# Optimization experiments

Hardware: AMD Instinct MI355X
Metric: run time of the kernel (lower is better)

## Reference

```python
import jax, jax.numpy as jnp
import numpy as np

B, N, K = 2, 8192, 9
IN_CH, FEAT_CH, COST_CH = 64, 128, 64

def _bn(x, p, eps=1e-5):
    # eval-mode BatchNorm; p is [4, C] = (gamma, beta, running_mean, running_var)
    sh = (1, -1) + (1,) * (x.ndim - 2)
    g, b, m, v = (p[i].reshape(sh) for i in range(4))
    return (x - m) / jnp.sqrt(v + eps) * g + b

def _c1(x, w, b):
    # Conv1d kernel 1: x [B,C,N], w [O,C]
    return jnp.einsum('oc,bcn->bon', w, x) + b[None, :, None]

def _forward(xyz, points, cost_volume, feats, flow,
             w0, b0, bn0, w1, b1, bn1,
             wz, bz, wr, br, wq, bq,
             w2a, b2a, w2b, b2b, wfc, bfc,
             rw0, rbn0, rw1, rbn1, rw2, rbn2,
             cw0, cbn0, cw1, cbn1, cw2, cbn2):
    lrelu = lambda t: jax.nn.leaky_relu(t, 0.1)
    # --- self-KNN on xyz ---
    xt = jnp.transpose(xyz, (0, 2, 1))                   # B N 3
    sq = jnp.sum(xt * xt, -1)                            # B N
    d2 = sq[:, :, None] + sq[:, None, :] - 2.0 * jnp.einsum('bnd,bmd->bnm', xt, xt)
    idx = jax.lax.top_k(-d2, K)[1]                       # B N K (nearest incl. self)
    # --- grouping_operation: gather neighbor features ---
    np0 = jnp.concatenate([cost_volume, flow], 1)        # B (cost_ch+3) N
    g = jax.vmap(lambda p, i: p[:, i])(np0, idx)         # B C N K
    # --- Conv2d(1x1)+BN+LeakyReLU stack ---
    g = lrelu(_bn(jnp.einsum('oc,bcnk->bonk', w0, g) + b0[None, :, None, None], bn0))
    g = lrelu(_bn(jnp.einsum('oc,bcnk->bonk', w1, g) + b1[None, :, None, None], bn1))
    h = jnp.max(g, -1)                                   # max over neighbors -> B 128 N
    # --- ConvGRU(x=feats, h) with 1x1 Conv1d gates ---
    hx = jnp.concatenate([h, feats], 1)
    z = jax.nn.sigmoid(_c1(hx, wz, bz))
    r = jax.nn.sigmoid(_c1(hx, wr, br))
    q = jnp.tanh(_c1(jnp.concatenate([r * h, feats], 1), wq, bq))
    h = (1.0 - z) * h + z * q
    # --- Conv1d MLP head ---
    x = jnp.concatenate([points, h], 1)                  # B (in_ch+128) N
    x = lrelu(_c1(x, w2a, b2a))
    x = lrelu(_c1(x, w2b, b2b))
    re_flow = _c1(x, wfc, bfc)                           # B 3 N
    # --- prob regnets (Conv1d no-bias + BN + ReLU) ---
    def reg(y, ws, ps):
        for w, p in zip(ws, ps):
            y = jax.nn.relu(_bn(jnp.einsum('oc,bcn->bon', w, y), p))
        return y
    refine = reg(x, [rw0, rw1, rw2], [rbn0, rbn1, rbn2])         # B 1 N
    coarse = reg(cost_volume, [cw0, cw1, cw2], [cbn0, cbn1, cbn2])
    re_flow = coarse * flow + refine * re_flow
    return x, jnp.clip(re_flow, -20.0, 20.0)

def setup_inputs():
    key = jax.random.key(0)
    ks = iter(jax.random.split(key, 80))
    nrm = lambda shape, s=1.0: jax.random.normal(next(ks), shape, jnp.float32) * s
    def bnp(C):
        g = jax.random.uniform(next(ks), (C,), jnp.float32) + 0.5
        b = nrm((C,), 0.1); m = nrm((C,), 0.1)
        v = jax.random.uniform(next(ks), (C,), jnp.float32) + 0.5
        return jnp.stack([g, b, m, v])
    z = lambda C: jnp.zeros((C,), jnp.float32)
    return dict(
        xyz=nrm((B, 3, N)), points=nrm((B, IN_CH, N)), cost_volume=nrm((B, COST_CH, N)),
        feats=nrm((B, FEAT_CH, N)), flow=nrm((B, 3, N), 0.1),
        w0=nrm((128, COST_CH + 3), 0.05), b0=z(128), bn0=bnp(128),
        w1=nrm((128, 128), 0.05), b1=z(128), bn1=bnp(128),
        wz=nrm((128, 256), 0.05), bz=z(128), wr=nrm((128, 256), 0.05), br=z(128),
        wq=nrm((128, 256), 0.05), bq=z(128),
        w2a=nrm((128, IN_CH + 128), 0.05), b2a=z(128), w2b=nrm((64, 128), 0.05), b2b=z(64),
        wfc=nrm((3, 64), 0.05), bfc=z(3),
        rw0=nrm((64, 64), 0.05), rbn0=bnp(64), rw1=nrm((64, 64), 0.05), rbn1=bnp(64),
        rw2=nrm((1, 64), 0.05), rbn2=bnp(1),
        cw0=nrm((64, COST_CH), 0.05), cbn0=bnp(64), cw1=nrm((64, 64), 0.05), cbn1=bnp(64),
        cw2=nrm((1, 64), 0.05), cbn2=bnp(1),
    )

def reference(xyz, points, cost_volume, feats, flow, w0, b0, bn0, w1, b1, bn1, wz, bz, wr, br, wq, bq, w2a, b2a, w2b, b2b, wfc, bfc, rw0, rbn0, rw1, rbn1, rw2, rbn2, cw0, cbn0, cw1, cbn1, cw2, cbn2):
    return _forward(xyz, points, cost_volume, feats, flow, w0, b0, bn0, w1, b1, bn1, wz, bz, wr, br, wq, bq, w2a, b2a, w2b, b2b, wfc, bfc, rw0, rbn0, rw1, rbn1, rw2, rbn2, cw0, cbn0, cw1, cbn1, cw2, cbn2)
```

## Files before the change

### kernel.cpp

```cpp
#include <hip/hip_runtime.h>
#include <math.h>

typedef __bf16 bf16;
typedef __bf16 bf16x4 __attribute__((ext_vector_type(4)));
typedef __bf16 bf16x8 __attribute__((ext_vector_type(8)));
typedef float f32x4 __attribute__((ext_vector_type(4)));

#define NPTS 8192
#define MTOT 16384

static __device__ __forceinline__ float b2f(bf16 x) { return (float)x; }
static __device__ __forceinline__ bf16  f2b(float x) { return (bf16)x; }

__global__ void diag_k(float* out, float code)
{
    if (threadIdx.x == 0 && blockIdx.x == 0) out[0] = code;
}

static __device__ __forceinline__ void pack_body(bf16 (*tile)[68],
                                                 const float* __restrict__ src, int Csrc,
                                                 bf16* __restrict__ dst, int ldd,
                                                 int nb, int cb, int b)
{
    const int t = threadIdx.x;
#pragma unroll
    for (int i = 0; i < 8; ++i) {
        int id = t + i * 256;
        int c = id >> 6, n = id & 63;
        int cc = cb + c;
        bf16 v = (bf16)0.0f;
        if (cc < Csrc) v = f2b(src[(size_t)(b * Csrc + cc) * NPTS + nb + n]);
        tile[c][n] = v;
    }
    __syncthreads();
#pragma unroll
    for (int i = 0; i < 8; ++i) {
        int id = t + i * 256;
        int n = id >> 5, c = id & 31;
        dst[(size_t)(b * NPTS + nb + n) * ldd + cb + c] = tile[c][n];
    }
}

static __device__ __forceinline__ float tau32(unsigned u)
{
    unsigned m = 0x80000000u | (unsigned)(~((int)u >> 31));
    return __uint_as_float(u ^ m);
}

static __device__ __forceinline__ unsigned dpp_shr1_u(unsigned x)
{
    return (unsigned)__builtin_amdgcn_update_dpp(0, (int)x, 0x111, 0xf, 0xf, true);
}
static __device__ __forceinline__ int dpp_shr1_i(int x)
{
    return __builtin_amdgcn_update_dpp(0, x, 0x111, 0xf, 0xf, true);
}

static __device__ __forceinline__ void mm32(
    f32x4 (&acc)[2][2],
    const bf16* A1, int lda1, int row01, int K1,
    const bf16* A2, int lda2, int row02,
    const bf16* W, int ldw, int K, int ob)
{
    const int lane = threadIdx.x & 63;
    const int q = lane >> 4, r = lane & 15;
    const bf16* Wp = W + (size_t)(ob + r) * ldw + q * 8;
    for (int k = 0; k < K; k += 32) {
        const bf16* Ap; int ld;
        if (k < K1) { ld = lda1; Ap = A1 + (size_t)(row01 + r) * lda1 + q * 8 + k; }
        else        { ld = lda2; Ap = A2 + (size_t)(row02 + r) * lda2 + q * 8 + (k - K1); }
        bf16x8 bv0 = *(const bf16x8*)(Wp + k);
        bf16x8 bv1 = *(const bf16x8*)(Wp + 16 * ldw + k);
        bf16x8 a0 = *(const bf16x8*)(Ap);
        bf16x8 a1 = *(const bf16x8*)(Ap + 16 * ld);
        acc[0][0] = __builtin_amdgcn_mfma_f32_16x16x32_bf16(a0, bv0, acc[0][0], 0, 0, 0);
        acc[1][0] = __builtin_amdgcn_mfma_f32_16x16x32_bf16(a1, bv0, acc[1][0], 0, 0, 0);
        acc[0][1] = __builtin_amdgcn_mfma_f32_16x16x32_bf16(a0, bv1, acc[0][1], 0, 0, 0);
        acc[1][1] = __builtin_amdgcn_mfma_f32_16x16x32_bf16(a1, bv1, acc[1][1], 0, 0, 0);
    }
}

static __device__ __forceinline__ void mm32x2(
    f32x4 (&acc)[2][2], f32x4 (&acc2)[2][2],
    const bf16* A1, int lda1, int row01, int K1,
    const bf16* A2, int lda2, int row02,
    const bf16* Wa, const bf16* Wb, int ldw, int K, int ob)
{
    const int lane = threadIdx.x & 63;
    const int q = lane >> 4, r = lane & 15;
    const bf16* Wpa = Wa + (size_t)(ob + r) * ldw + q * 8;
    const bf16* Wpb = Wb + (size_t)(ob + r) * ldw + q * 8;
    for (int k = 0; k < K; k += 32) {
        const bf16* Ap; int ld;
        if (k < K1) { ld = lda1; Ap = A1 + (size_t)(row01 + r) * lda1 + q * 8 + k; }
        else        { ld = lda2; Ap = A2 + (size_t)(row02 + r) * lda2 + q * 8 + (k - K1); }
        bf16x8 a0 = *(const bf16x8*)(Ap);
        bf16x8 a1 = *(const bf16x8*)(Ap + 16 * ld);
        bf16x8 ba0 = *(const bf16x8*)(Wpa + k);
        bf16x8 ba1 = *(const bf16x8*)(Wpa + 16 * ldw + k);
        bf16x8 bb0 = *(const bf16x8*)(Wpb + k);
        bf16x8 bb1 = *(const bf16x8*)(Wpb + 16 * ldw + k);
        acc[0][0]  = __builtin_amdgcn_mfma_f32_16x16x32_bf16(a0, ba0, acc[0][0], 0, 0, 0);
        acc[1][0]  = __builtin_amdgcn_mfma_f32_16x16x32_bf16(a1, ba0, acc[1][0], 0, 0, 0);
        acc[0][1]  = __builtin_amdgcn_mfma_f32_16x16x32_bf16(a0, ba1, acc[0][1], 0, 0, 0);
        acc[1][1]  = __builtin_amdgcn_mfma_f32_16x16x32_bf16(a1, ba1, acc[1][1], 0, 0, 0);
        acc2[0][0] = __builtin_amdgcn_mfma_f32_16x16x32_bf16(a0, bb0, acc2[0][0], 0, 0, 0);
        acc2[1][0] = __builtin_amdgcn_mfma_f32_16x16x32_bf16(a1, bb0, acc2[1][0], 0, 0, 0);
        acc2[0][1] = __builtin_amdgcn_mfma_f32_16x16x32_bf16(a0, bb1, acc2[0][1], 0, 0, 0);
        acc2[1][1] = __builtin_amdgcn_mfma_f32_16x16x32_bf16(a1, bb1, acc2[1][1], 0, 0, 0);
    }
}

static __device__ __forceinline__ void zacc(f32x4 (&acc)[2][2])
{
    f32x4 z = {0.f, 0.f, 0.f, 0.f};
    acc[0][0] = z; acc[0][1] = z; acc[1][0] = z; acc[1][1] = z;
}

__global__ __launch_bounds__(256) void pack_a(
    const float* __restrict__ w0, const float* __restrict__ w1,
    const float* __restrict__ wz, const float* __restrict__ wr,
    const float* __restrict__ wq, const float* __restrict__ w2a,
    const float* __restrict__ w2b, const float* __restrict__ rw0,
    const float* __restrict__ rw1, const float* __restrict__ cw0,
    const float* __restrict__ cw1,
    const float* __restrict__ cost, const float* __restrict__ flow,
    bf16* __restrict__ w0p, bf16* __restrict__ wts,
    bf16* __restrict__ CV, bf16* __restrict__ FL)
{
    __shared__ __align__(16) bf16 tile[32][68];
    const int bx = blockIdx.x;
    if (bx < 48) {
        int id = bx * 256 + threadIdx.x;
        if (id < 128 * 96) {
            int o = id / 96, c = id - o * 96;
            w0p[id] = (c < 67) ? f2b(w0[o * 67 + c]) : (bf16)0.0f;
        }
    } else if (bx < 688) {
        int id = (bx - 48) * 256 + threadIdx.x;
        if (id < 163840) {
            const float* s; int off;
            if (id < 16384)       { s = w1;  off = 0; }
            else if (id < 49152)  { s = wz;  off = 16384; }
            else if (id < 81920)  { s = wr;  off = 49152; }
            else if (id < 114688) { s = wq;  off = 81920; }
            else if (id < 139264) { s = w2a; off = 114688; }
            else if (id < 147456) { s = w2b; off = 139264; }
            else if (id < 151552) { s = rw0; off = 147456; }
            else if (id < 155648) { s = rw1; off = 151552; }
            else if (id < 159744) { s = cw0; off = 155648; }
            else                  { s = cw1; off = 159744; }
            wts[id] = f2b(s[id - off]);
        }
    } else if (bx < 1200) {
        int l = bx - 688, x = l & 127, r2 = l >> 7;
        pack_body(tile, cost, 64, CV, 64, x * 64, (r2 & 1) * 32, r2 >> 1);
    } else {
        int l = bx - 1200, x = l & 127, b = l >> 7;
        pack_body(tile, flow, 3, FL, 32, x * 64, 0, b);
    }
}

__global__ __launch_bounds__(256, 5) void knn_conv_packb(
    const float* __restrict__ xyz, const float* __restrict__ feats,
    const float* __restrict__ points,
    const bf16* __restrict__ CV, const bf16* __restrict__ FL,
    const bf16* __restrict__ W0p, const bf16* __restrict__ W1,
    const float* __restrict__ b0, const float* __restrict__ bn0,
    const float* __restrict__ b1, const float* __restrict__ bn1,
    bf16* __restrict__ FE, bf16* __restrict__ PT,
    bf16* __restrict__ P2, int* __restrict__ idxg)
{
    __shared__ __align__(16) char smem[16384];
    const int bx = blockIdx.x;
    if (bx < 4096) {
        float4* pts = (float4*)smem;
        const int t = threadIdx.x, lane = t & 63, w = t >> 6;
        const int qid = bx * 4 + w, b = qid >> 13;
        const float* X = xyz + b * 3 * NPTS;
        const int n = qid & (NPTS - 1);
        const float qx = X[n], qy = X[NPTS + n], qz = X[2 * NPTS + n];
        const float qsq = qx * qx + qy * qy + qz * qz;

        unsigned kkd = 0xFFFFFFFFu;
        int      idd = 0;
        float tau = __builtin_inff();

        for (int ch = 0; ch < 8; ++ch) {
            __syncthreads();
#pragma unroll
            for (int r2 = 0; r2 < 4; ++r2) {
                int i2 = t + r2 * 256;
                int ci = ch * 1024 + i2;
                float x = X[ci], y = X[NPTS + ci], z = X[2 * NPTS + ci];
                pts[i2] = make_float4(x, y, z, x * x + y * y + z * z);
            }
            __syncthreads();
            int i0 = 0;
            if (ch == 0) {
                float4 c = pts[lane];
                float d = (qsq + c.w) - 2.0f * (qx * c.x + qy * c.y + qz * c.z);
                unsigned kd = __float_as_uint(d);
                kd ^= ((unsigned)((int)kd >> 31)) | 0x80000000u;
                unsigned long long key = ((unsigned long long)kd << 32) | (unsigned)lane;
#pragma unroll
                for (int r = 0; r < 9; ++r) {
                    unsigned long long m = key;
#pragma unroll
                    for (int s = 1; s < 64; s <<= 1) {
                        unsigned long long o = __shfl_xor(m, s);
                        if (o < m) m = o;
                    }
                    if (lane == r) {
                        kkd = (unsigned)(m >> 32);
                        idd = (int)(unsigned)(m & 0xffffffffu);
                    }
                    if (key == m) key = ~0ull;
                }
                tau = tau32((unsigned)__builtin_amdgcn_readlane((int)kkd, 8));
                i0 = 1;
            }
            for (int i = i0; i < 16; ++i) {
                float4 c = pts[i * 64 + lane];
                float d = (qsq + c.w) - 2.0f * (qx * c.x + qy * c.y + qz * c.z);
                unsigned long long mask = __ballot(d <= tau);
                if (mask) {
                    const int base = ch * 1024 + i * 64;
                    do {
                        int L = __builtin_ctzll(mask);
                        mask &= mask - 1;
                        unsigned di = (unsigned)__builtin_amdgcn_readlane(
                                          __float_as_int(d), L);
                        unsigned kd = di ^ (((unsigned)((int)di >> 31)) | 0x80000000u);
                        const int idxn = base + L;
                        unsigned kprev = dpp_shr1_u(kkd);
                        int      iprev = dpp_shr1_i(idd);
                        bool lt  = kd < kkd;
                        bool ltp = kd < kprev;
                        kkd = lt ? (ltp ? kprev : kd)   : kkd;
                        idd = lt ? (ltp ? iprev : idxn) : idd;
                    } while (mask);
                    tau = tau32((unsigned)__builtin_amdgcn_readlane((int)kkd, 8));
                }
            }
        }
        if (lane < 9) {
            int m = idd;
            m = ((unsigned)m < (unsigned)NPTS) ? m : 0;
            idxg[qid * 9 + lane] = b * NPTS + m;
        }
    } else if (bx < 4608) {
        bf16 (*P1t)[136] = (bf16 (*)[136])smem;
        const int w = threadIdx.x >> 6, lane = threadIdx.x & 63;
        const int q = lane >> 4, r = lane & 15;
        const int ptb = (bx - 4096) * 32;
        {
            f32x4 acc[2][2]; zacc(acc);
            const int ob = w * 32;
            mm32(acc, CV, 64, ptb, 64, FL, 32, ptb, W0p, 96, 96, ob);
#pragma unroll
            for (int to = 0; to < 2; ++to) {
                const int o = ob + to * 16 + r;
                float bs = b0[o];
                float gg = bn0[o], be = bn0[128 + o], mm = bn0[256 + o];
                float rs = 1.0f / sqrtf(bn0[384 + o] + 1e-5f);
#pragma unroll
                for (int tm = 0; tm < 2; ++tm) {
#pragma unroll
                    for (int rr = 0; rr < 4; ++rr) {
                        const int jl = tm * 16 + q * 4 + rr;
                        float v = acc[tm][to][rr] + bs;
                        v = (v - mm) * rs * gg + be;
                        v = v > 0.f ? v : 0.1f * v;
                        P1t[jl][o] = f2b(v);
                    }
                }
            }
        }
        __syncthreads();
        {
            f32x4 acc[2][2]; zacc(acc);
            const int ob = w * 32;
            mm32(acc, &P1t[0][0], 136, 0, 128, &P1t[0][0], 136, 0, W1, 128, 128, ob);
#pragma unroll
            for (int to = 0; to < 2; ++to) {
                const int o = ob + to * 16 + r;
                float bs = b1[o];
                float gg = bn1[o], be = bn1[128 + o], mm = bn1[256 + o];
                float rs = 1.0f / sqrtf(bn1[384 + o] + 1e-5f);
#pragma unroll
                for (int tm = 0; tm < 2; ++tm) {
#pragma unroll
                    for (int rr = 0; rr < 4; ++rr) {
                        const int jl = tm * 16 + q * 4 + rr;
                        float v = acc[tm][to][rr] + bs;
                        v = (v - mm) * rs * gg + be;
                        v = v > 0.f ? v : 0.1f * v;
                        P2[(size_t)(ptb + jl) * 128 + o] = f2b(v);
                    }
                }
            }
        }
    } else if (bx < 5632) {
        bf16 (*tile)[68] = (bf16 (*)[68])smem;
        int l = bx - 4608, x = l & 127, r2 = l >> 7;
        pack_body(tile, feats, 128, FE, 128, x * 64, (r2 & 3) * 32, r2 >> 2);
    } else {
        bf16 (*tile)[68] = (bf16 (*)[68])smem;
        int l = bx - 5632, x = l & 127, r2 = l >> 7;
        pack_body(tile, points, 64, PT, 64, x * 64, (r2 & 1) * 32, r2 >> 1);
    }
}

struct MRP {
    const bf16 *P2, *FE, *PT, *CV;
    const int  *idx;
    const bf16 *WZ, *WR, *WQ, *W2A, *W2B, *RW0, *RW1, *CW0, *CW1;
    const float *bz, *br, *bq, *b2a, *b2b;
    const float *rbn0, *rbn1, *cbn0, *cbn1;
    const float *rw2, *rbn2, *cw2, *cbn2, *wfc, *bfc, *flow;
    float* out;
};

__global__ __launch_bounds__(256) void megarow(MRP p)
{
    __shared__ __align__(16) bf16 Zt[32][136], RHt[32][136], HPt[32][136], X1t[32][136];
    __shared__ __align__(16) bf16 X2t[32][72], R1t[32][72], R2t[32][72],
                                  C1t[32][72], C2t[32][72];
    __shared__ int idxt[32][9];
    const int w = threadIdx.x >> 6, lane = threadIdx.x & 63;
    const int q = lane >> 4, r = lane & 15;
    const int ptb = blockIdx.x * 32;

    for (int id = threadIdx.x; id < 288; id += 256) {
        int jl = id / 9, k = id - jl * 9;
        int m = p.idx[(ptb + jl) * 9 + k];
        idxt[jl][k] = ((unsigned)m < (unsigned)MTOT) ? m : 0;
    }
    __syncthreads();
    {
        const int c4 = (threadIdx.x & 31) * 4;
        const int jr = threadIdx.x >> 5;
#pragma unroll
        for (int jj = 0; jj < 4; ++jj) {
            const int jl = jr + 8 * jj;
            float mx0 = -__builtin_inff(), mx1 = -__builtin_inff();
            float mx2 = -__builtin_inff(), mx3 = -__builtin_inff();
#pragma unroll
            for (int k = 0; k < 9; ++k) {
                bf16x4 v = *(const bf16x4*)(p.P2 + (size_t)idxt[jl][k] * 128 + c4);
                mx0 = fmaxf(mx0, b2f(v[0]));
                mx1 = fmaxf(mx1, b2f(v[1]));
                mx2 = fmaxf(mx2, b2f(v[2]));
                mx3 = fmaxf(mx3, b2f(v[3]));
            }
            bf16x4 st;
            st[0] = f2b(mx0); st[1] = f2b(mx1); st[2] = f2b(mx2); st[3] = f2b(mx3);
            *(bf16x4*)&X1t[jl][c4] = st;
        }
    }
    __syncthreads();

    {
        const int ob = w * 32;
        f32x4 acc[2][2], acc2[2][2]; zacc(acc); zacc(acc2);
        mm32x2(acc, acc2, &X1t[0][0], 136, 0, 128, p.FE, 128, ptb,
               p.WZ, p.WR, 256, 256, ob);
#pragma unroll
        for (int to = 0; to < 2; ++to) {
            const int o = ob + to * 16 + r;
            const float bs = p.bz[o];
#pragma unroll
            for (int tm = 0; tm < 2; ++tm)
#pragma unroll
                for (int rr = 0; rr < 4; ++rr) {
                    const int jl = tm * 16 + q * 4 + rr;
                    float v = acc[tm][to][rr] + bs;
                    Zt[jl][o] = f2b(1.0f / (1.0f + expf(-v)));
                }
        }
#pragma unroll
        for (int to = 0; to < 2; ++to) {
            const int o = ob + to * 16 + r;
            const float bs = p.br[o];
#pragma unroll
            for (int tm = 0; tm < 2; ++tm)
#pragma unroll
                for (int rr = 0; rr < 4; ++rr) {
                    const int jl = tm * 16 + q * 4 + rr;
                    float v = acc2[tm][to][rr] + bs;
                    v = 1.0f / (1.0f + expf(-v));
                    RHt[jl][o] = f2b(v * b2f(X1t[jl][o]));
                }
        }
    }
    __syncthreads();
    {
        const int ob = w * 32;
        f32x4 acc[2][2]; zacc(acc);
        mm32(acc, &RHt[0][0], 136, 0, 128, p.FE, 128, ptb, p.WQ, 256, 256, ob);
#pragma unroll
        for (int to = 0; to < 2; ++to) {
            const int o = ob + to * 16 + r;
            const float bs = p.bq[o];
#pragma unroll
            for (int tm = 0; tm < 2; ++tm)
#pragma unroll
                for (int rr = 0; rr < 4; ++rr) {
                    const int jl = tm * 16 + q * 4 + rr;
                    float v = acc[tm][to][rr] + bs;
                    float qv = tanhf(v);
                    float z = b2f(Zt[jl][o]);
                    float h = b2f(X1t[jl][o]);
                    HPt[jl][o] = f2b((1.0f - z) * h + z * qv);
                }
        }
    }
    __syncthreads();
    {
        const int ob = w * 32;
        f32x4 acc[2][2]; zacc(acc);
        mm32(acc, p.PT, 64, ptb, 64, &HPt[0][0], 136, 0, p.W2A, 192, 192, ob);
#pragma unroll
        for (int to = 0; to < 2; ++to) {
            const int o = ob + to * 16 + r;
            const float bs = p.b2a[o];
#pragma unroll
            for (int tm = 0; tm < 2; ++tm)
#pragma unroll
                for (int rr = 0; rr < 4; ++rr) {
                    const int jl = tm * 16 + q * 4 + rr;
                    float v = acc[tm][to][rr] + bs;
                    X1t[jl][o] = f2b(v > 0.f ? v : 0.1f * v);
                }
        }
    }
    __syncthreads();
    if (w < 2) {
        const int ob = w * 32;
        f32x4 acc[2][2]; zacc(acc);
        mm32(acc, &X1t[0][0], 136, 0, 128, &X1t[0][0], 136, 0, p.W2B, 128, 128, ob);
#pragma unroll
        for (int to = 0; to < 2; ++to) {
            const int o = ob + to * 16 + r;
            const float bs = p.b2b[o];
#pragma unroll
            for (int tm = 0; tm < 2; ++tm)
#pragma unroll
                for (int rr = 0; rr < 4; ++rr) {
                    const int jl = tm * 16 + q * 4 + rr;
                    float v = acc[tm][to][rr] + bs;
                    v = v > 0.f ? v : 0.1f * v;
                    X2t[jl][o] = f2b(v);
                    const int j = ptb + jl, bb = j >> 13, nn = j & (NPTS - 1);
                    p.out[(size_t)bb * 64 * NPTS + (size_t)o * NPTS + nn] = v;
                }
        }
    } else {
        const int ob = (w - 2) * 32;
        f32x4 acc[2][2]; zacc(acc);
        mm32(acc, p.CV, 64, ptb, 64, p.CV, 64, ptb, p.CW0, 64, 64, ob);
#pragma unroll
        for (int to = 0; to < 2; ++to) {
            const int o = ob + to * 16 + r;
            float gg = p.cbn0[o], be = p.cbn0[64 + o], mm = p.cbn0[128 + o];
            float rs = 1.0f / sqrtf(p.cbn0[192 + o] + 1e-5f);
#pragma unroll
            for (int tm = 0; tm < 2; ++tm)
#pragma unroll
                for (int rr = 0; rr < 4; ++rr) {
                    const int jl = tm * 16 + q * 4 + rr;
                    float v = acc[tm][to][rr];
                    v = (v - mm) * rs * gg + be;
                    C1t[jl][o] = f2b(fmaxf(v, 0.f));
                }
        }
    }
    __syncthreads();
    if (w < 2) {
        const int ob = w * 32;
        f32x4 acc[2][2]; zacc(acc);
        mm32(acc, &X2t[0][0], 72, 0, 64, &X2t[0][0], 72, 0, p.RW0, 64, 64, ob);
#pragma unroll
        for (int to = 0; to < 2; ++to) {
            const int o = ob + to * 16 + r;
            float gg = p.rbn0[o], be = p.rbn0[64 + o], mm = p.rbn0[128 + o];
            float rs = 1.0f / sqrtf(p.rbn0[192 + o] + 1e-5f);
#pragma unroll
            for (int tm = 0; tm < 2; ++tm)
#pragma unroll
                for (int rr = 0; rr < 4; ++rr) {
                    const int jl = tm * 16 + q * 4 + rr;
                    float v = acc[tm][to][rr];
                    v = (v - mm) * rs * gg + be;
                    R1t[jl][o] = f2b(fmaxf(v, 0.f));
                }
        }
    } else {
        const int ob = (w - 2) * 32;
        f32x4 acc[2][2]; zacc(acc);
        mm32(acc, &C1t[0][0], 72, 0, 64, &C1t[0][0], 72, 0, p.CW1, 64, 64, ob);
#pragma unroll
        for (int to = 0; to < 2; ++to) {
            const int o = ob + to * 16 + r;
            float gg = p.cbn1[o], be = p.cbn1[64 + o], mm = p.cbn1[128 + o];
            float rs = 1.0f / sqrtf(p.cbn1[192 + o] + 1e-5f);
#pragma unroll
            for (int tm = 0; tm < 2; ++tm)
#pragma unroll
                for (int rr = 0; rr < 4; ++rr) {
                    const int jl = tm * 16 + q * 4 + rr;
                    float v = acc[tm][to][rr];
                    v = (v - mm) * rs * gg + be;
                    C2t[jl][o] = f2b(fmaxf(v, 0.f));
                }
        }
    }
    __syncthreads();
    if (w < 2) {
        const int ob = w * 32;
        f32x4 acc[2][2]; zacc(acc);
        mm32(acc, &R1t[0][0], 72, 0, 64, &R1t[0][0], 72, 0, p.RW1, 64, 64, ob);
#pragma unroll
        for (int to = 0; to < 2; ++to) {
            const int o = ob + to * 16 + r;
            float gg = p.rbn1[o], be = p.rbn1[64 + o], mm = p.rbn1[128 + o];
            float rs = 1.0f / sqrtf(p.rbn1[192 + o] + 1e-5f);
#pragma unroll
            for (int tm = 0; tm < 2; ++tm)
#pragma unroll
                for (int rr = 0; rr < 4; ++rr) {
                    const int jl = tm * 16 + q * 4 + rr;
                    float v = acc[tm][to][rr];
                    v = (v - mm) * rs * gg + be;
                    R2t[jl][o] = f2b(fmaxf(v, 0.f));
                }
        }
    }
    __syncthreads();
    if (threadIdx.x < 32) {
        const int jl = threadIdx.x, j = ptb + jl;
        const int b = j >> 13, n = j & (NPTS - 1);
        float dr = 0.f, dc = 0.f, p0 = 0.f, p1 = 0.f, p2 = 0.f;
#pragma unroll
        for (int c = 0; c < 64; ++c) {
            float x = b2f(X2t[jl][c]);
            dr += p.rw2[c] * b2f(R2t[jl][c]);
            dc += p.cw2[c] * b2f(C2t[jl][c]);
            p0 += p.wfc[c] * x;
            p1 += p.wfc[64 + c] * x;
            p2 += p.wfc[128 + c] * x;
        }
        float refine = (dr - p.rbn2[2]) / sqrtf(p.rbn2[3] + 1e-5f) * p.rbn2[0] + p.rbn2[1];
        refine = fmaxf(refine, 0.f);
        float coarse = (dc - p.cbn2[2]) / sqrtf(p.cbn2[3] + 1e-5f) * p.cbn2[0] + p.cbn2[1];
        coarse = fmaxf(coarse, 0.f);
        p0 += p.bfc[0]; p1 += p.bfc[1]; p2 += p.bfc[2];
        const float f0 = p.flow[(size_t)b * 3 * NPTS + n];
        const float f1 = p.flow[(size_t)b * 3 * NPTS + NPTS + n];
        const float f2v = p.flow[(size_t)b * 3 * NPTS + 2 * NPTS + n];
        float o0 = fminf(fmaxf(coarse * f0 + refine * p0, -20.f), 20.f);
        float o1 = fminf(fmaxf(coarse * f1 + refine * p1, -20.f), 20.f);
        float o2 = fminf(fmaxf(coarse * f2v + refine * p2, -20.f), 20.f);
        float* ro = p.out + 1048576;
        ro[(size_t)b * 3 * NPTS + n] = o0;
        ro[(size_t)b * 3 * NPTS + NPTS + n] = o1;
        ro[(size_t)b * 3 * NPTS + 2 * NPTS + n] = o2;
    }
}

extern "C" void kernel_launch(void* const* d_in, const int* in_sizes, int n_in,
                              void* d_out, int out_size, void* d_ws, size_t ws_size,
                              hipStream_t stream)
{
    static const int EXP[35] = {
        49152, 1048576, 1048576, 2097152, 49152,
        8576, 128, 512, 16384, 128, 512,
        32768, 128, 32768, 128, 32768, 128,
        24576, 128, 8192, 64, 192, 3,
        4096, 256, 4096, 256, 64, 4,
        4096, 256, 4096, 256, 64, 4 };
    float code = 0.f;
    if (n_in != 35) code = 900.f;
    else if (out_size != 1097728) code = 950.f;
    else if (ws_size < 18767872u) code = 980.f;
    else { for (int i = 0; i < 35; ++i) if (in_sizes[i] != EXP[i]) { code = 1000.f + 4.f * i; break; } }
    if (code != 0.f) { diag_k<<<dim3(1), dim3(64), 0, stream>>>((float*)d_out, code); return; }

    const float* xyz    = (const float*)d_in[0];
    const float* points = (const float*)d_in[1];
    const float* cost   = (const float*)d_in[2];
    const float* feats  = (const float*)d_in[3];
    const float* flow   = (const float*)d_in[4];
    const float* w0     = (const float*)d_in[5];
    const float* b0     = (const float*)d_in[6];
    const float* bn0    = (const float*)d_in[7];
    const float* w1     = (const float*)d_in[8];
    const float* b1     = (const float*)d_in[9];
    const float* bn1    = (const float*)d_in[10];
    const float* wz     = (const float*)d_in[11];
    const float* bz     = (const float*)d_in[12];
    const float* wr     = (const float*)d_in[13];
    const float* br     = (const float*)d_in[14];
    const float* wq     = (const float*)d_in[15];
    const float* bq     = (const float*)d_in[16];
    const float* w2a    = (const float*)d_in[17];
    const float* b2a    = (const float*)d_in[18];
    const float* w2b    = (const float*)d_in[19];
    const float* b2b    = (const float*)d_in[20];
    const float* wfc    = (const float*)d_in[21];
    const float* bfc    = (const float*)d_in[22];
    const float* rw0    = (const float*)d_in[23];
    const float* rbn0   = (const float*)d_in[24];
    const float* rw1    = (const float*)d_in[25];
    const float* rbn1   = (const float*)d_in[26];
    const float* rw2    = (const float*)d_in[27];
    const float* rbn2   = (const float*)d_in[28];
    const float* cw0    = (const float*)d_in[29];
    const float* cbn0   = (const float*)d_in[30];
    const float* cw1    = (const float*)d_in[31];
    const float* cbn1   = (const float*)d_in[32];
    const float* cw2    = (const float*)d_in[33];
    const float* cbn2   = (const float*)d_in[34];

    char* ws = (char*)d_ws;
    bf16* W0p  = (bf16*)(ws + 0);
    bf16* WTS  = (bf16*)(ws + 24576);
    int*  idxg = (int*) (ws + 352256);
    bf16* CV   = (bf16*)(ws + 942080);
    bf16* FL   = (bf16*)(ws + 3039232);
    bf16* FE   = (bf16*)(ws + 4087808);
    bf16* PT   = (bf16*)(ws + 8282112);
    bf16* P2   = (bf16*)(ws + 10379264);

    bf16* W1  = WTS;
    bf16* WZ  = WTS + 16384;
    bf16* WR  = WTS + 49152;
    bf16* WQ  = WTS + 81920;
    bf16* W2A = WTS + 114688;
    bf16* W2B = WTS + 139264;
    bf16* RW0 = WTS + 147456;
    bf16* RW1 = WTS + 151552;
    bf16* CW0 = WTS + 155648;
    bf16* CW1 = WTS + 159744;

    float* out = (float*)d_out;

     pack_a<<<dim3(1456), dim3(256), 0, stream>>>(
              w0, w1, wz, wr, wq, w2a, w2b, rw0, rw1, cw0, cw1,
              cost, flow, W0p, WTS, CV, FL);
     knn_conv_packb<<<dim3(6144), dim3(256), 0, stream>>>(
              xyz, feats, points, CV, FL, W0p, W1, b0, bn0, b1, bn1,
              FE, PT, P2, idxg);
     MRP mp;
          mp.P2 = P2; mp.FE = FE; mp.PT = PT; mp.CV = CV; mp.idx = idxg;
          mp.WZ = WZ; mp.WR = WR; mp.WQ = WQ; mp.W2A = W2A; mp.W2B = W2B;
          mp.RW0 = RW0; mp.RW1 = RW1; mp.CW0 = CW0; mp.CW1 = CW1;
          mp.bz = bz; mp.br = br; mp.bq = bq; mp.b2a = b2a; mp.b2b = b2b;
          mp.rbn0 = rbn0; mp.rbn1 = rbn1; mp.cbn0 = cbn0; mp.cbn1 = cbn1;
          mp.rw2 = rw2; mp.rbn2 = rbn2; mp.cw2 = cw2; mp.cbn2 = cbn2;
          mp.wfc = wfc; mp.bfc = bfc; mp.flow = flow; mp.out = out;
          megarow<<<dim3(512), dim3(256), 0, stream>>>(mp);

    (void)n_in;
}
```

Before: 245.3 us.

## Move coarse regnet into KNN kernel and widen megarow blocks to 512 threads

The coarse-probability branch (CW0/CW1/cw2 with BN+ReLU) moves out of the megarow kernel into 256 extra blocks of knn_conv_packb. Those blocks write a per-point coarse scalar to workspace, and megarow reads it back. Megarow now launches 512 threads, with each wave handling 16 output channels instead of 32. The intent is to shorten megarow's serial dependency chain and give it more waves per block. The cost is extra blocks in the KNN kernel, a small global round trip, and more waves idle in the 64-channel stages.

```diff
diff --git a/kernel.cpp b/kernel.cpp
--- a/kernel.cpp
+++ b/kernel.cpp
@@ -80,8 +80,35 @@
     }
 }
 
-static __device__ __forceinline__ void mm32x2(
-    f32x4 (&acc)[2][2], f32x4 (&acc2)[2][2],
+static __device__ __forceinline__ void zacc(f32x4 (&acc)[2][2])
+{
+    f32x4 z = {0.f, 0.f, 0.f, 0.f};
+    acc[0][0] = z; acc[0][1] = z; acc[1][0] = z; acc[1][1] = z;
+}
+
+static __device__ __forceinline__ void mm16(
+    f32x4 (&acc)[2],
+    const bf16* A1, int lda1, int row01, int K1,
+    const bf16* A2, int lda2, int row02,
+    const bf16* W, int ldw, int K, int ob)
+{
+    const int lane = threadIdx.x & 63;
+    const int q = lane >> 4, r = lane & 15;
+    const bf16* Wp = W + (size_t)(ob + r) * ldw + q * 8;
+    for (int k = 0; k < K; k += 32) {
+        const bf16* Ap; int ld;
+        if (k < K1) { ld = lda1; Ap = A1 + (size_t)(row01 + r) * lda1 + q * 8 + k; }
+        else        { ld = lda2; Ap = A2 + (size_t)(row02 + r) * lda2 + q * 8 + (k - K1); }
+        bf16x8 bv0 = *(const bf16x8*)(Wp + k);
+        bf16x8 a0 = *(const bf16x8*)(Ap);
+        bf16x8 a1 = *(const bf16x8*)(Ap + 16 * ld);
+        acc[0] = __builtin_amdgcn_mfma_f32_16x16x32_bf16(a0, bv0, acc[0], 0, 0, 0);
+        acc[1] = __builtin_amdgcn_mfma_f32_16x16x32_bf16(a1, bv0, acc[1], 0, 0, 0);
+    }
+}
+
+static __device__ __forceinline__ void mm16x2(
+    f32x4 (&acc)[2], f32x4 (&acc2)[2],
     const bf16* A1, int lda1, int row01, int K1,
     const bf16* A2, int lda2, int row02,
     const bf16* Wa, const bf16* Wb, int ldw, int K, int ob)
@@ -97,24 +124,18 @@
         bf16x8 a0 = *(const bf16x8*)(Ap);
         bf16x8 a1 = *(const bf16x8*)(Ap + 16 * ld);
         bf16x8 ba0 = *(const bf16x8*)(Wpa + k);
-        bf16x8 ba1 = *(const bf16x8*)(Wpa + 16 * ldw + k);
         bf16x8 bb0 = *(const bf16x8*)(Wpb + k);
-        bf16x8 bb1 = *(const bf16x8*)(Wpb + 16 * ldw + k);
-        acc[0][0]  = __builtin_amdgcn_mfma_f32_16x16x32_bf16(a0, ba0, acc[0][0], 0, 0, 0);
-        acc[1][0]  = __builtin_amdgcn_mfma_f32_16x16x32_bf16(a1, ba0, acc[1][0], 0, 0, 0);
-        acc[0][1]  = __builtin_amdgcn_mfma_f32_16x16x32_bf16(a0, ba1, acc[0][1], 0, 0, 0);
-        acc[1][1]  = __builtin_amdgcn_mfma_f32_16x16x32_bf16(a1, ba1, acc[1][1], 0, 0, 0);
-        acc2[0][0] = __builtin_amdgcn_mfma_f32_16x16x32_bf16(a0, bb0, acc2[0][0], 0, 0, 0);
-        acc2[1][0] = __builtin_amdgcn_mfma_f32_16x16x32_bf16(a1, bb0, acc2[1][0], 0, 0, 0);
-        acc2[0][1] = __builtin_amdgcn_mfma_f32_16x16x32_bf16(a0, bb1, acc2[0][1], 0, 0, 0);
-        acc2[1][1] = __builtin_amdgcn_mfma_f32_16x16x32_bf16(a1, bb1, acc2[1][1], 0, 0, 0);
-    }
-}
-
-static __device__ __forceinline__ void zacc(f32x4 (&acc)[2][2])
+        acc[0]  = __builtin_amdgcn_mfma_f32_16x16x32_bf16(a0, ba0, acc[0], 0, 0, 0);
+        acc[1]  = __builtin_amdgcn_mfma_f32_16x16x32_bf16(a1, ba0, acc[1], 0, 0, 0);
+        acc2[0] = __builtin_amdgcn_mfma_f32_16x16x32_bf16(a0, bb0, acc2[0], 0, 0, 0);
+        acc2[1] = __builtin_amdgcn_mfma_f32_16x16x32_bf16(a1, bb0, acc2[1], 0, 0, 0);
+    }
+}
+
+static __device__ __forceinline__ void zacc2(f32x4 (&acc)[2])
 {
     f32x4 z = {0.f, 0.f, 0.f, 0.f};
-    acc[0][0] = z; acc[0][1] = z; acc[1][0] = z; acc[1][1] = z;
+    acc[0] = z; acc[1] = z;
 }
 
 __global__ __launch_bounds__(256) void pack_a(
@@ -166,12 +187,16 @@
     const float* __restrict__ points,
     const bf16* __restrict__ CV, const bf16* __restrict__ FL,
     const bf16* __restrict__ W0p, const bf16* __restrict__ W1,
+    const bf16* __restrict__ CW0, const bf16* __restrict__ CW1,
     const float* __restrict__ b0, const float* __restrict__ bn0,
     const float* __restrict__ b1, const float* __restrict__ bn1,
+    const float* __restrict__ cbn0, const float* __restrict__ cbn1,
+    const float* __restrict__ cw2, const float* __restrict__ cbn2,
     bf16* __restrict__ FE, bf16* __restrict__ PT,
-    bf16* __restrict__ P2, int* __restrict__ idxg)
-{
-    __shared__ __align__(16) char smem[16384];
+    bf16* __restrict__ P2, int* __restrict__ idxg,
+    float* __restrict__ coarseG)
+{
+    __shared__ __align__(16) char smem[18432];
     const int bx = blockIdx.x;
     if (bx < 4096) {
         float4* pts = (float4*)smem;
@@ -305,35 +330,91 @@
         bf16 (*tile)[68] = (bf16 (*)[68])smem;
         int l = bx - 4608, x = l & 127, r2 = l >> 7;
         pack_body(tile, feats, 128, FE, 128, x * 64, (r2 & 3) * 32, r2 >> 2);
-    } else {
+    } else if (bx < 6144) {
         bf16 (*tile)[68] = (bf16 (*)[68])smem;
         int l = bx - 5632, x = l & 127, r2 = l >> 7;
         pack_body(tile, points, 64, PT, 64, x * 64, (r2 & 1) * 32, r2 >> 1);
+    } else {
+        bf16 (*C1t)[72] = (bf16 (*)[72])smem;
+        bf16 (*C2t)[72] = (bf16 (*)[72])(smem + 9216);
+        const int w = threadIdx.x >> 6, lane = threadIdx.x & 63;
+        const int q = lane >> 4, r = lane & 15;
+        const int row0 = (w >> 1) * 32;
+        const int pt0 = (bx - 6144) * 64 + row0;
+        const int ob = (w & 1) * 32;
+        {
+            f32x4 acc[2][2]; zacc(acc);
+            mm32(acc, CV, 64, pt0, 64, CV, 64, pt0, CW0, 64, 64, ob);
+#pragma unroll
+            for (int to = 0; to < 2; ++to) {
+                const int o = ob + to * 16 + r;
+                float gg = cbn0[o], be = cbn0[64 + o], mm = cbn0[128 + o];
+                float rs = 1.0f / sqrtf(cbn0[192 + o] + 1e-5f);
+#pragma unroll
+                for (int tm = 0; tm < 2; ++tm)
+#pragma unroll
+                    for (int rr = 0; rr < 4; ++rr) {
+                        const int jl = tm * 16 + q * 4 + rr;
+                        float v = acc[tm][to][rr];
+                        v = (v - mm) * rs * gg + be;
+                        C1t[row0 + jl][o] = f2b(fmaxf(v, 0.f));
+                    }
+            }
+        }
+        __syncthreads();
+        {
+            f32x4 acc[2][2]; zacc(acc);
+            mm32(acc, &C1t[0][0], 72, row0, 64, &C1t[0][0], 72, row0, CW1, 64, 64, ob);
+#pragma unroll
+            for (int to = 0; to < 2; ++to) {
+                const int o = ob + to * 16 + r;
+                float gg = cbn1[o], be = cbn1[64 + o], mm = cbn1[128 + o];
+                float rs = 1.0f / sqrtf(cbn1[192 + o] + 1e-5f);
+#pragma unroll
+                for (int tm = 0; tm < 2; ++tm)
+#pragma unroll
+                    for (int rr = 0; rr < 4; ++rr) {
+                        const int jl = tm * 16 + q * 4 + rr;
+                        float v = acc[tm][to][rr];
+                        v = (v - mm) * rs * gg + be;
+                        C2t[row0 + jl][o] = f2b(fmaxf(v, 0.f));
+                    }
+            }
+        }
+        __syncthreads();
+        if (threadIdx.x < 64) {
+            const int jl = threadIdx.x;
+            const int j = (bx - 6144) * 64 + jl;
+            float dc = 0.f;
+#pragma unroll
+            for (int c = 0; c < 64; ++c) dc += cw2[c] * b2f(C2t[jl][c]);
+            float coarse = (dc - cbn2[2]) / sqrtf(cbn2[3] + 1e-5f) * cbn2[0] + cbn2[1];
+            coarseG[j] = fmaxf(coarse, 0.f);
+        }
     }
 }
 
 struct MRP {
-    const bf16 *P2, *FE, *PT, *CV;
+    const bf16 *P2, *FE, *PT;
     const int  *idx;
-    const bf16 *WZ, *WR, *WQ, *W2A, *W2B, *RW0, *RW1, *CW0, *CW1;
+    const bf16 *WZ, *WR, *WQ, *W2A, *W2B, *RW0, *RW1;
     const float *bz, *br, *bq, *b2a, *b2b;
-    const float *rbn0, *rbn1, *cbn0, *cbn1;
-    const float *rw2, *rbn2, *cw2, *cbn2, *wfc, *bfc, *flow;
+    const float *rbn0, *rbn1;
+    const float *rw2, *rbn2, *wfc, *bfc, *flow, *coarse;
     float* out;
 };
 
-__global__ __launch_bounds__(256) void megarow(MRP p)
+__global__ __launch_bounds__(512) void megarow(MRP p)
 {
     __shared__ __align__(16) bf16 Zt[32][136], RHt[32][136], HPt[32][136], X1t[32][136];
-    __shared__ __align__(16) bf16 X2t[32][72], R1t[32][72], R2t[32][72],
-                                  C1t[32][72], C2t[32][72];
+    __shared__ __align__(16) bf16 X2t[32][72], R1t[32][72], R2t[32][72];
     __shared__ int idxt[32][9];
     const int w = threadIdx.x >> 6, lane = threadIdx.x & 63;
     const int q = lane >> 4, r = lane & 15;
     const int ptb = blockIdx.x * 32;
 
-    for (int id = threadIdx.x; id < 288; id += 256) {
-        int jl = id / 9, k = id - jl * 9;
+    if (threadIdx.x < 288) {
+        int jl = threadIdx.x / 9, k = threadIdx.x - jl * 9;
         int m = p.idx[(ptb + jl) * 9 + k];
         idxt[jl][k] = ((unsigned)m < (unsigned)MTOT) ? m : 0;
     }
@@ -342,8 +423,8 @@
         const int c4 = (threadIdx.x & 31) * 4;
         const int jr = threadIdx.x >> 5;
 #pragma unroll
-        for (int jj = 0; jj < 4; ++jj) {
-            const int jl = jr + 8 * jj;
+        for (int jj = 0; jj < 2; ++jj) {
+            const int jl = jr + 16 * jj;
             float mx0 = -__builtin_inff(), mx1 = -__builtin_inff();
             float mx2 = -__builtin_inff(), mx3 = -__builtin_inff();
 #pragma unroll
@@ -362,199 +443,137 @@
     __syncthreads();
 
     {
-        const int ob = w * 32;
-        f32x4 acc[2][2], acc2[2][2]; zacc(acc); zacc(acc2);
-        mm32x2(acc, acc2, &X1t[0][0], 136, 0, 128, p.FE, 128, ptb,
+        const int ob = w * 16;
+        f32x4 acc[2], acc2[2]; zacc2(acc); zacc2(acc2);
+        mm16x2(acc, acc2, &X1t[0][0], 136, 0, 128, p.FE, 128, ptb,
                p.WZ, p.WR, 256, 256, ob);
-#pragma unroll
-        for (int to = 0; to < 2; ++to) {
-            const int o = ob + to * 16 + r;
-            const float bs = p.bz[o];
-#pragma unroll
-            for (int tm = 0; tm < 2; ++tm)
-#pragma unroll
-                for (int rr = 0; rr < 4; ++rr) {
-                    const int jl = tm * 16 + q * 4 + rr;
-                    float v = acc[tm][to][rr] + bs;
-                    Zt[jl][o] = f2b(1.0f / (1.0f + expf(-v)));
-                }
-        }
-#pragma unroll
-        for (int to = 0; to < 2; ++to) {
-            const int o = ob + to * 16 + r;
-            const float bs = p.br[o];
-#pragma unroll
-            for (int tm = 0; tm < 2; ++tm)
-#pragma unroll
-                for (int rr = 0; rr < 4; ++rr) {
-                    const int jl = tm * 16 + q * 4 + rr;
-                    float v = acc2[tm][to][rr] + bs;
-                    v = 1.0f / (1.0f + expf(-v));
-                    RHt[jl][o] = f2b(v * b2f(X1t[jl][o]));
-                }
-        }
+        const int o = ob + r;
+        const float bsz = p.bz[o];
+#pragma unroll
+        for (int tm = 0; tm < 2; ++tm)
+#pragma unroll
+            for (int rr = 0; rr < 4; ++rr) {
+                const int jl = tm * 16 + q * 4 + rr;
+                float v = acc[tm][rr] + bsz;
+                Zt[jl][o] = f2b(1.0f / (1.0f + expf(-v)));
+            }
+        const float bsr = p.br[o];
+#pragma unroll
+        for (int tm = 0; tm < 2; ++tm)
+#pragma unroll
+            for (int rr = 0; rr < 4; ++rr) {
+                const int jl = tm * 16 + q * 4 + rr;
+                float v = acc2[tm][rr] + bsr;
+                v = 1.0f / (1.0f + expf(-v));
+                RHt[jl][o] = f2b(v * b2f(X1t[jl][o]));
+            }
     }
     __syncthreads();
     {
-        const int ob = w * 32;
-        f32x4 acc[2][2]; zacc(acc);
-        mm32(acc, &RHt[0][0], 136, 0, 128, p.FE, 128, ptb, p.WQ, 256, 256, ob);
-#pragma unroll
-        for (int to = 0; to < 2; ++to) {
-            const int o = ob + to * 16 + r;
-            const float bs = p.bq[o];
-#pragma unroll
-            for (int tm = 0; tm < 2; ++tm)
-#pragma unroll
-                for (int rr = 0; rr < 4; ++rr) {
-                    const int jl = tm * 16 + q * 4 + rr;
-                    float v = acc[tm][to][rr] + bs;
-                    float qv = tanhf(v);
-                    float z = b2f(Zt[jl][o]);
-                    float h = b2f(X1t[jl][o]);
-                    HPt[jl][o] = f2b((1.0f - z) * h + z * qv);
-                }
-        }
+        const int ob = w * 16;
+        f32x4 acc[2]; zacc2(acc);
+        mm16(acc, &RHt[0][0], 136, 0, 128, p.FE, 128, ptb, p.WQ, 256, 256, ob);
+        const int o = ob + r;
+        const float bs = p.bq[o];
+#pragma unroll
+        for (int tm = 0; tm < 2; ++tm)
+#pragma unroll
+            for (int rr = 0; rr < 4; ++rr) {
+                const int jl = tm * 16 + q * 4 + rr;
+                float v = acc[tm][rr] + bs;
+                float qv = tanhf(v);
+                float z = b2f(Zt[jl][o]);
+                float h = b2f(X1t[jl][o]);
+                HPt[jl][o] = f2b((1.0f - z) * h + z * qv);
+            }
     }
     __syncthreads();
     {
-        const int ob = w * 32;
-        f32x4 acc[2][2]; zacc(acc);
-        mm32(acc, p.PT, 64, ptb, 64, &HPt[0][0], 136, 0, p.W2A, 192, 192, ob);
-#pragma unroll
-        for (int to = 0; to < 2; ++to) {
-            const int o = ob + to * 16 + r;
-            const float bs = p.b2a[o];
-#pragma unroll
-            for (int tm = 0; tm < 2; ++tm)
-#pragma unroll
-                for (int rr = 0; rr < 4; ++rr) {
-                    const int jl = tm * 16 + q * 4 + rr;
-                    float v = acc[tm][to][rr] + bs;
-                    X1t[jl][o] = f2b(v > 0.f ? v : 0.1f * v);
-                }
-        }
-    }
-    __syncthreads();
-    if (w < 2) {
-        const int ob = w * 32;
-        f32x4 acc[2][2]; zacc(acc);
-        mm32(acc, &X1t[0][0], 136, 0, 128, &X1t[0][0], 136, 0, p.W2B, 128, 128, ob);
-#pragma unroll
-        for (int to = 0; to < 2; ++to) {
-            const int o = ob + to * 16 + r;
-            const float bs = p.b2b[o];
-#pragma unroll
-            for (int tm = 0; tm < 2; ++tm)
-#pragma unroll
-                for (int rr = 0; rr < 4; ++rr) {
-                    const int jl = tm * 16 + q * 4 + rr;
-                    float v = acc[tm][to][rr] + bs;
-                    v = v > 0.f ? v : 0.1f * v;
-                    X2t[jl][o] = f2b(v);
-                    const int j = ptb + jl, bb = j >> 13, nn = j & (NPTS - 1);
-                    p.out[(size_t)bb * 64 * NPTS + (size_t)o * NPTS + nn] = v;
-                }
-        }
-    } else {
-        const int ob = (w - 2) * 32;
-        f32x4 acc[2][2]; zacc(acc);
-        mm32(acc, p.CV, 64, ptb, 64, p.CV, 64, ptb, p.CW0, 64, 64, ob);
-#pragma unroll
-        for (int to = 0; to < 2; ++to) {
-            const int o = ob + to * 16 + r;
-            float gg = p.cbn0[o], be = p.cbn0[64 + o], mm = p.cbn0[128 + o];
-            float rs = 1.0f / sqrtf(p.cbn0[192 + o] + 1e-5f);
-#pragma unroll
-            for (int tm = 0; tm < 2; ++tm)
-#pragma unroll
-                for (int rr = 0; rr < 4; ++rr) {
-                    const int jl = tm * 16 + q * 4 + rr;
-                    float v = acc[tm][to][rr];
-                    v = (v - mm) * rs * gg + be;
-                    C1t[jl][o] = f2b(fmaxf(v, 0.f));
-                }
-        }
-    }
-    __syncthreads();
-    if (w < 2) {
-        const int ob = w * 32;
-        f32x4 acc[2][2]; zacc(acc);
-        mm32(acc, &X2t[0][0], 72, 0, 64, &X2t[0][0], 72, 0, p.RW0, 64, 64, ob);
-#pragma unroll
-        for (int to = 0; to < 2; ++to) {
-            const int o = ob + to * 16 + r;
-            float gg = p.rbn0[o], be = p.rbn0[64 + o], mm = p.rbn0[128 + o];
-            float rs = 1.0f / sqrtf(p.rbn0[192 + o] + 1e-5f);
-#pragma unroll
-            for (int tm = 0; tm < 2; ++tm)
-#pragma unroll
-                for (int rr = 0; rr < 4; ++rr) {
-                    const int jl = tm * 16 + q * 4 + rr;
-                    float v = acc[tm][to][rr];
-                    v = (v - mm) * rs * gg + be;
-                    R1t[jl][o] = f2b(fmaxf(v, 0.f));
-                }
-        }
-    } else {
-        const int ob = (w - 2) * 32;
-        f32x4 acc[2][2]; zacc(acc);
-        mm32(acc, &C1t[0][0], 72, 0, 64, &C1t[0][0], 72, 0, p.CW1, 64, 64, ob);
-#pragma unroll
-        for (int to = 0; to < 2; ++to) {
-            const int o = ob + to * 16 + r;
-            float gg = p.cbn1[o], be = p.cbn1[64 + o], mm = p.cbn1[128 + o];
-            float rs = 1.0f / sqrtf(p.cbn1[192 + o] + 1e-5f);
-#pragma unroll
-            for (int tm = 0; tm < 2; ++tm)
-#pragma unroll
-                for (int rr = 0; rr < 4; ++rr) {
-                    const int jl = tm * 16 + q * 4 + rr;
-                    float v = acc[tm][to][rr];
-                    v = (v - mm) * rs * gg + be;
-                    C2t[jl][o] = f2b(fmaxf(v, 0.f));
-                }
-        }
-    }
-    __syncthreads();
-    if (w < 2) {
-        const int ob = w * 32;
-        f32x4 acc[2][2]; zacc(acc);
-        mm32(acc, &R1t[0][0], 72, 0, 64, &R1t[0][0], 72, 0, p.RW1, 64, 64, ob);
-#pragma unroll
-        for (int to = 0; to < 2; ++to) {
-            const int o = ob + to * 16 + r;
-            float gg = p.rbn1[o], be = p.rbn1[64 + o], mm = p.rbn1[128 + o];
-            float rs = 1.0f / sqrtf(p.rbn1[192 + o] + 1e-5f);
-#pragma unroll
-            for (int tm = 0; tm < 2; ++tm)
-#pragma unroll
-                for (int rr = 0; rr < 4; ++rr) {
-                    const int jl = tm * 16 + q * 4 + rr;
-                    float v = acc[tm][to][rr];
-                    v = (v - mm) * rs * gg + be;
-                    R2t[jl][o] = f2b(fmaxf(v, 0.f));
-                }
-        }
+        const int ob = w * 16;
+        f32x4 acc[2]; zacc2(acc);
+        mm16(acc, p.PT, 64, ptb, 64, &HPt[0][0], 136, 0, p.W2A, 192, 192, ob);
+        const int o = ob + r;
+        const float bs = p.b2a[o];
+#pragma unroll
+        for (int tm = 0; tm < 2; ++tm)
+#pragma unroll
+            for (int rr = 0; rr < 4; ++rr) {
+                const int jl = tm * 16 + q * 4 + rr;
+                float v = acc[tm][rr] + bs;
+                X1t[jl][o] = f2b(v > 0.f ? v : 0.1f * v);
+            }
+    }
+    __syncthreads();
+    if (w < 4) {
+        const int ob = w * 16;
+        f32x4 acc[2]; zacc2(acc);
+        mm16(acc, &X1t[0][0], 136, 0, 128, &X1t[0][0], 136, 0, p.W2B, 128, 128, ob);
+        const int o = ob + r;
+        const float bs = p.b2b[o];
+#pragma unroll
+        for (int tm = 0; tm < 2; ++tm)
+#pragma unroll
+            for (int rr = 0; rr < 4; ++rr) {
+                const int jl = tm * 16 + q * 4 + rr;
+                float v = acc[tm][rr] + bs;
+                v = v > 0.f ? v : 0.1f * v;
+                X2t[jl][o] = f2b(v);
+                const int j = ptb + jl, bb = j >> 13, nn = j & (NPTS - 1);
+                p.out[(size_t)bb * 64 * NPTS + (size_t)o * NPTS + nn] = v;
+            }
+    }
+    __syncthreads();
+    if (w < 4) {
+        const int ob = w * 16;
+        f32x4 acc[2]; zacc2(acc);
+        mm16(acc, &X2t[0][0], 72, 0, 64, &X2t[0][0], 72, 0, p.RW0, 64, 64, ob);
+        const int o = ob + r;
+        float gg = p.rbn0[o], be = p.rbn0[64 + o], mm = p.rbn0[128 + o];
+        float rs = 1.0f / sqrtf(p.rbn0[192 + o] + 1e-5f);
+#pragma unroll
+        for (int tm = 0; tm < 2; ++tm)
+#pragma unroll
+            for (int rr = 0; rr < 4; ++rr) {
+                const int jl = tm * 16 + q * 4 + rr;
+                float v = acc[tm][rr];
+                v = (v - mm) * rs * gg + be;
+                R1t[jl][o] = f2b(fmaxf(v, 0.f));
+            }
+    }
+    __syncthreads();
+    if (w < 4) {
+        const int ob = w * 16;
+        f32x4 acc[2]; zacc2(acc);
+        mm16(acc, &R1t[0][0], 72, 0, 64, &R1t[0][0], 72, 0, p.RW1, 64, 64, ob);
+        const int o = ob + r;
+        float gg = p.rbn1[o], be = p.rbn1[64 + o], mm = p.rbn1[128 + o];
+        float rs = 1.0f / sqrtf(p.rbn1[192 + o] + 1e-5f);
+#pragma unroll
+        for (int tm = 0; tm < 2; ++tm)
+#pragma unroll
+            for (int rr = 0; rr < 4; ++rr) {
+                const int jl = tm * 16 + q * 4 + rr;
+                float v = acc[tm][rr];
+                v = (v - mm) * rs * gg + be;
+                R2t[jl][o] = f2b(fmaxf(v, 0.f));
+            }
     }
     __syncthreads();
     if (threadIdx.x < 32) {
         const int jl = threadIdx.x, j = ptb + jl;
         const int b = j >> 13, n = j & (NPTS - 1);
-        float dr = 0.f, dc = 0.f, p0 = 0.f, p1 = 0.f, p2 = 0.f;
+        float dr = 0.f, p0 = 0.f, p1 = 0.f, p2 = 0.f;
 #pragma unroll
         for (int c = 0; c < 64; ++c) {
             float x = b2f(X2t[jl][c]);
             dr += p.rw2[c] * b2f(R2t[jl][c]);
-            dc += p.cw2[c] * b2f(C2t[jl][c]);
             p0 += p.wfc[c] * x;
             p1 += p.wfc[64 + c] * x;
             p2 += p.wfc[128 + c] * x;
         }
         float refine = (dr - p.rbn2[2]) / sqrtf(p.rbn2[3] + 1e-5f) * p.rbn2[0] + p.rbn2[1];
         refine = fmaxf(refine, 0.f);
-        float coarse = (dc - p.cbn2[2]) / sqrtf(p.cbn2[3] + 1e-5f) * p.cbn2[0] + p.cbn2[1];
-        coarse = fmaxf(coarse, 0.f);
+        const float coarse = p.coarse[j];
         p0 += p.bfc[0]; p1 += p.bfc[1]; p2 += p.bfc[2];
         const float f0 = p.flow[(size_t)b * 3 * NPTS + n];
         const float f1 = p.flow[(size_t)b * 3 * NPTS + NPTS + n];
@@ -624,14 +643,15 @@
     const float* cbn2   = (const float*)d_in[34];
 
     char* ws = (char*)d_ws;
-    bf16* W0p  = (bf16*)(ws + 0);
-    bf16* WTS  = (bf16*)(ws + 24576);
-    int*  idxg = (int*) (ws + 352256);
-    bf16* CV   = (bf16*)(ws + 942080);
-    bf16* FL   = (bf16*)(ws + 3039232);
-    bf16* FE   = (bf16*)(ws + 4087808);
-    bf16* PT   = (bf16*)(ws + 8282112);
-    bf16* P2   = (bf16*)(ws + 10379264);
+    bf16*  W0p  = (bf16*)(ws + 0);
+    bf16*  WTS  = (bf16*)(ws + 24576);
+    int*   idxg = (int*) (ws + 352256);
+    bf16*  CV   = (bf16*)(ws + 942080);
+    bf16*  FL   = (bf16*)(ws + 3039232);
+    bf16*  FE   = (bf16*)(ws + 4087808);
+    bf16*  PT   = (bf16*)(ws + 8282112);
+    bf16*  P2   = (bf16*)(ws + 10379264);
+    float* CO   = (float*)(ws + 14573568);
 
     bf16* W1  = WTS;
     bf16* WZ  = WTS + 16384;
@@ -649,18 +669,20 @@
      pack_a<<<dim3(1456), dim3(256), 0, stream>>>(
               w0, w1, wz, wr, wq, w2a, w2b, rw0, rw1, cw0, cw1,
               cost, flow, W0p, WTS, CV, FL);
-     knn_conv_packb<<<dim3(6144), dim3(256), 0, stream>>>(
-              xyz, feats, points, CV, FL, W0p, W1, b0, bn0, b1, bn1,
-              FE, PT, P2, idxg);
+     knn_conv_packb<<<dim3(6400), dim3(256), 0, stream>>>(
+              xyz, feats, points, CV, FL, W0p, W1, CW0, CW1,
+              b0, bn0, b1, bn1, cbn0, cbn1, cw2, cbn2,
+              FE, PT, P2, idxg, CO);
      MRP mp;
-          mp.P2 = P2; mp.FE = FE; mp.PT = PT; mp.CV = CV; mp.idx = idxg;
+          mp.P2 = P2; mp.FE = FE; mp.PT = PT; mp.idx = idxg;
           mp.WZ = WZ; mp.WR = WR; mp.WQ = WQ; mp.W2A = W2A; mp.W2B = W2B;
-          mp.RW0 = RW0; mp.RW1 = RW1; mp.CW0 = CW0; mp.CW1 = CW1;
+          mp.RW0 = RW0; mp.RW1 = RW1;
           mp.bz = bz; mp.br = br; mp.bq = bq; mp.b2a = b2a; mp.b2b = b2b;
-          mp.rbn0 = rbn0; mp.rbn1 = rbn1; mp.cbn0 = cbn0; mp.cbn1 = cbn1;
-          mp.rw2 = rw2; mp.rbn2 = rbn2; mp.cw2 = cw2; mp.cbn2 = cbn2;
-          mp.wfc = wfc; mp.bfc = bfc; mp.flow = flow; mp.out = out;
-          megarow<<<dim3(512), dim3(256), 0, stream>>>(mp);
+          mp.rbn0 = rbn0; mp.rbn1 = rbn1;
+          mp.rw2 = rw2; mp.rbn2 = rbn2;
+          mp.wfc = wfc; mp.bfc = bfc; mp.flow = flow; mp.coarse = CO;
+          mp.out = out;
+          megarow<<<dim3(512), dim3(512), 0, stream>>>(mp);
 
     (void)n_in;
 }
```

Result: no change. 242.6 us (-1.1%).
